# Performance work log

Hardware: AMD Instinct MI355X
Metric: run time of the kernel (lower is better)

Reference implementation:

```python
import jax, jax.numpy as jnp
import numpy as np

B, N, D_NODE, D_GRAPH = 512, 512, 128, 128
EPS = 1e-12  # torch F.normalize eps


def setup_inputs() -> dict:
    key = jax.random.key(0)
    k_h, k_ns, k_wf, k_bf, k_wg, k_bg = jax.random.split(key, 6)
    s = 1.0 / np.sqrt(D_NODE)
    return {
        "h": jax.random.normal(k_h, (B, N, D_NODE), dtype=jnp.float32),
        "ns": jax.random.randint(k_ns, (B,), 1, N + 1, dtype=jnp.int64),
        "W_f": jax.random.uniform(k_wf, (D_GRAPH, D_NODE), jnp.float32, -s, s),
        "b_f": jax.random.uniform(k_bf, (D_GRAPH,), jnp.float32, -s, s),
        "W_g": jax.random.uniform(k_wg, (1, D_NODE), jnp.float32, -s, s),
        "b_g": jax.random.uniform(k_bg, (1,), jnp.float32, -s, s),
    }


def reference(h, ns, W_f, b_f, W_g, b_g):
    # h: [B, N, D_node]; ns: [B] valid node counts per graph
    h_vG = jnp.einsum("bnd,ed->bne", h, W_f) + b_f          # [B, N, D_graph]
    g_vG = jax.nn.sigmoid(jnp.einsum("bnd,od->bno", h, W_g) + b_g)  # [B, N, 1]
    mask = (jnp.arange(N) < ns[:, None])[:, :, None]         # [B, N, 1]
    h_G = jnp.sum(h_vG * g_vG * mask, axis=1)                # [B, D_graph]
    norm = jnp.linalg.norm(h_G, axis=-1, keepdims=True)
    return h_G / jnp.maximum(norm, EPS)
```

## Files before the change

kernel.cpp:

```cpp
#include <hip/hip_runtime.h>
#include <math.h>

#define BB 512
#define NN 512
#define DD 128

__global__ __launch_bounds__(512) void k_graph(
    const float* __restrict__ h,
    const int*   __restrict__ ns,
    const float* __restrict__ W_g,
    const float* __restrict__ b_g,
    const float* __restrict__ W_f,
    const float* __restrict__ b_f,
    float*       __restrict__ out)
{
    const int b    = blockIdx.x;
    const int tid  = threadIdx.x;
    const int grp  = tid >> 5;
    const int lane = tid & 31;

    const int end = ns[b];

    __shared__ float lds_s[16 * 128];
    __shared__ float lds_t[16];
    __shared__ float red[2];

    const float4 wg = ((const float4*)W_g)[lane];
    const float  bg = b_g[0];
    const float4* hb = (const float4*)(h + (size_t)b * NN * DD);

    float4 acc  = make_float4(0.f, 0.f, 0.f, 0.f);
    float  tacc = 0.f;

    int n = grp;
    for (; n + 48 < end; n += 64) {
        const float4 v0 = hb[(size_t)(n     ) * 32 + lane];
        const float4 v1 = hb[(size_t)(n + 16) * 32 + lane];
        const float4 v2 = hb[(size_t)(n + 32) * 32 + lane];
        const float4 v3 = hb[(size_t)(n + 48) * 32 + lane];

        float d0 = v0.x * wg.x + v0.y * wg.y + v0.z * wg.z + v0.w * wg.w;
        float d1 = v1.x * wg.x + v1.y * wg.y + v1.z * wg.z + v1.w * wg.w;
        float d2 = v2.x * wg.x + v2.y * wg.y + v2.z * wg.z + v2.w * wg.w;
        float d3 = v3.x * wg.x + v3.y * wg.y + v3.z * wg.z + v3.w * wg.w;
        #pragma unroll
        for (int m = 1; m <= 16; m <<= 1) {
            d0 += __shfl_xor(d0, m);
            d1 += __shfl_xor(d1, m);
            d2 += __shfl_xor(d2, m);
            d3 += __shfl_xor(d3, m);
        }
        const float g0 = 1.f / (1.f + expf(-(d0 + bg)));
        const float g1 = 1.f / (1.f + expf(-(d1 + bg)));
        const float g2 = 1.f / (1.f + expf(-(d2 + bg)));
        const float g3 = 1.f / (1.f + expf(-(d3 + bg)));

        acc.x += g0 * v0.x + g1 * v1.x + g2 * v2.x + g3 * v3.x;
        acc.y += g0 * v0.y + g1 * v1.y + g2 * v2.y + g3 * v3.y;
        acc.z += g0 * v0.z + g1 * v1.z + g2 * v2.z + g3 * v3.z;
        acc.w += g0 * v0.w + g1 * v1.w + g2 * v2.w + g3 * v3.w;
        tacc  += g0 + g1 + g2 + g3;
    }
    for (; n < end; n += 16) {
        const float4 v = hb[(size_t)n * 32 + lane];
        float d = v.x * wg.x + v.y * wg.y + v.z * wg.z + v.w * wg.w;
        #pragma unroll
        for (int m = 1; m <= 16; m <<= 1) d += __shfl_xor(d, m);
        const float g = 1.f / (1.f + expf(-(d + bg)));
        acc.x += g * v.x;
        acc.y += g * v.y;
        acc.z += g * v.z;
        acc.w += g * v.w;
        tacc  += g;
    }

    ((float4*)lds_s)[grp * 32 + lane] = acc;
    if (lane == 0) lds_t[grp] = tacc;
    __syncthreads();

    float s = 0.f, t = 0.f;
    if (tid < 128) {
        #pragma unroll
        for (int g2 = 0; g2 < 16; ++g2) s += lds_s[g2 * 128 + tid];
        #pragma unroll
        for (int g2 = 0; g2 < 16; ++g2) t += lds_t[g2];
    }
    __syncthreads();
    if (tid < 128) lds_s[tid] = s;
    __syncthreads();

    float hg = 0.f;
    if (tid < 128) {
        hg = t * b_f[tid];
        const float4* wrow = (const float4*)(W_f + (size_t)tid * DD);
        const float4* sv   = (const float4*)lds_s;
        #pragma unroll 8
        for (int k = 0; k < 32; ++k) {
            const float4 w  = wrow[k];
            const float4 sk = sv[k];
            hg += w.x * sk.x + w.y * sk.y + w.z * sk.z + w.w * sk.w;
        }
        float sq = hg * hg;
        sq += __shfl_xor(sq, 1);
        sq += __shfl_xor(sq, 2);
        sq += __shfl_xor(sq, 4);
        sq += __shfl_xor(sq, 8);
        sq += __shfl_xor(sq, 16);
        sq += __shfl_xor(sq, 32);
        if ((tid & 63) == 0) red[tid >> 6] = sq;
    }
    __syncthreads();
    if (tid < 128) {
        const float norm = sqrtf(red[0] + red[1]);
        out[(size_t)b * DD + tid] = hg / fmaxf(norm, 1e-12f);
    }
}

extern "C" void kernel_launch(void* const* d_in, const int* in_sizes, int n_in,
                              void* d_out, int out_size, void* d_ws, size_t ws_size,
                              hipStream_t stream) {
    const float* h   = (const float*)d_in[0];
    const int*   ns  = (const int*)  d_in[1];
    const float* W_f = (const float*)d_in[2];
    const float* b_f = (const float*)d_in[3];
    const float* W_g = (const float*)d_in[4];
    const float* b_g = (const float*)d_in[5];
    float* out = (float*)d_out;

    k_graph<<<BB, 512, 0, stream>>>(h, ns, W_g, b_g, W_f, b_f, out);
}
```

Baseline: 24.76 us.

## Split each graph's node range across four blocks with last-block reduction

Each graph's nodes are split into four chunks handled by separate blocks, giving four times as many blocks. Each block writes its partial gated sums to a workspace and increments a per-graph atomic counter. The last block to arrive combines the partials and runs the W_f projection and normalization. The goal is better load balance and occupancy across CUs when graph sizes vary. In exchange it adds a memset launch, workspace traffic and an atomic handshake. The partial stores and the counter increment are relaxed atomics with no release/acquire fence, which could be a visibility risk.

```diff
diff --git a/kernel.cpp b/kernel.cpp
--- a/kernel.cpp
+++ b/kernel.cpp
@@ -4,26 +4,36 @@
 #define BB 512
 #define NN 512
 #define DD 128
+#define S_CHUNKS 4
+#define CHUNK (NN / S_CHUNKS)
+#define PSTRIDE 132
 
-__global__ __launch_bounds__(512) void k_graph(
+__global__ __launch_bounds__(512) void k_fused(
     const float* __restrict__ h,
     const int*   __restrict__ ns,
     const float* __restrict__ W_g,
     const float* __restrict__ b_g,
     const float* __restrict__ W_f,
     const float* __restrict__ b_f,
+    float*       __restrict__ part,
+    int*         __restrict__ cnt,
     float*       __restrict__ out)
 {
-    const int b    = blockIdx.x;
+    const int bc   = blockIdx.x;
+    const int b    = bc >> 2;
+    const int c    = bc & 3;
     const int tid  = threadIdx.x;
     const int grp  = tid >> 5;
     const int lane = tid & 31;
 
-    const int end = ns[b];
+    const int nsb   = ns[b];
+    const int start = c * CHUNK;
+    const int end   = min(start + CHUNK, nsb);
 
     __shared__ float lds_s[16 * 128];
     __shared__ float lds_t[16];
     __shared__ float red[2];
+    __shared__ int   last;
 
     const float4 wg = ((const float4*)W_g)[lane];
     const float  bg = b_g[0];
@@ -32,7 +42,7 @@
     float4 acc  = make_float4(0.f, 0.f, 0.f, 0.f);
     float  tacc = 0.f;
 
-    int n = grp;
+    int n = start + grp;
     for (; n + 48 < end; n += 64) {
         const float4 v0 = hb[(size_t)(n     ) * 32 + lane];
         const float4 v1 = hb[(size_t)(n + 16) * 32 + lane];
@@ -78,20 +88,48 @@
     if (lane == 0) lds_t[grp] = tacc;
     __syncthreads();
 
-    float s = 0.f, t = 0.f;
+    float* slot = part + (size_t)bc * PSTRIDE;
+    if (tid < 128) {
+        float s = 0.f;
+        #pragma unroll
+        for (int g2 = 0; g2 < 16; ++g2) s += lds_s[g2 * 128 + tid];
+        __hip_atomic_store(&slot[tid], s, __ATOMIC_RELAXED, __HIP_MEMORY_SCOPE_AGENT);
+    }
+    if (tid == 0) {
+        float t = 0.f;
+        #pragma unroll
+        for (int g2 = 0; g2 < 16; ++g2) t += lds_t[g2];
+        __hip_atomic_store(&slot[128], t, __ATOMIC_RELAXED, __HIP_MEMORY_SCOPE_AGENT);
+    }
+
+    __syncthreads();
+    if (tid == 0) {
+        const int old = __hip_atomic_fetch_add(&cnt[b], 1, __ATOMIC_RELAXED,
+                                               __HIP_MEMORY_SCOPE_AGENT);
+        last = (old == S_CHUNKS - 1);
+    }
+    __syncthreads();
+    if (!last) return;
+
+    const float* pb = part + (size_t)(b * S_CHUNKS) * PSTRIDE;
+    float s2 = 0.f, t2 = 0.f;
     if (tid < 128) {
         #pragma unroll
-        for (int g2 = 0; g2 < 16; ++g2) s += lds_s[g2 * 128 + tid];
+        for (int cc = 0; cc < S_CHUNKS; ++cc)
+            s2 += __hip_atomic_load(&pb[cc * PSTRIDE + tid], __ATOMIC_RELAXED,
+                                    __HIP_MEMORY_SCOPE_AGENT);
         #pragma unroll
-        for (int g2 = 0; g2 < 16; ++g2) t += lds_t[g2];
+        for (int cc = 0; cc < S_CHUNKS; ++cc)
+            t2 += __hip_atomic_load(&pb[cc * PSTRIDE + 128], __ATOMIC_RELAXED,
+                                    __HIP_MEMORY_SCOPE_AGENT);
     }
     __syncthreads();
-    if (tid < 128) lds_s[tid] = s;
+    if (tid < 128) lds_s[tid] = s2;
     __syncthreads();
 
     float hg = 0.f;
     if (tid < 128) {
-        hg = t * b_f[tid];
+        hg = t2 * b_f[tid];
         const float4* wrow = (const float4*)(W_f + (size_t)tid * DD);
         const float4* sv   = (const float4*)lds_s;
         #pragma unroll 8
@@ -127,5 +165,9 @@
     const float* b_g = (const float*)d_in[5];
     float* out = (float*)d_out;
 
-    k_graph<<<BB, 512, 0, stream>>>(h, ns, W_g, b_g, W_f, b_f, out);
+    float* part = (float*)d_ws;
+    int*   cnt  = (int*)(part + (size_t)BB * S_CHUNKS * PSTRIDE);
+
+    hipMemsetAsync(cnt, 0, BB * sizeof(int), stream);
+    k_fused<<<BB * S_CHUNKS, 512, 0, stream>>>(h, ns, W_g, b_g, W_f, b_f, part, cnt, out);
 }
```

New measurement: 36.91 us. 49.0% more time.
